# Kernel optimization log

Measured on AMD Instinct MI355X. Metric: run time of the kernel, lower is better.

Reference implementation:

```python
import jax, jax.numpy as jnp
import numpy as np

D = 192   # token_dim == channel_dim == expert_dim == adapt_dim (required by source code)
S = 4096  # sequence length
NE = 8    # num_experts


def _ln(x, g, b, eps=1e-5):
    m = x.mean(-1, keepdims=True)
    v = ((x - m) ** 2).mean(-1, keepdims=True)
    return (x - m) / jnp.sqrt(v + eps) * g + b


def _adaptive(x, a, W, b, AW, Ab):
    # AdaptiveLinear with adapt_method='add': weight = W + adapt(a).view(out, in)
    dW = (AW @ a + Ab).reshape(W.shape)
    return x @ (W + dW).T + b


def setup_inputs() -> dict:
    key = jax.random.key(0)
    ks = iter(jax.random.split(key, 40))

    def n(shape, s=0.05):
        return jax.random.normal(next(ks), shape, dtype=jnp.float32) * s

    return {
        "x": n((1, S, D), 1.0),
        "W_in": n((D, D)), "b_in": n((D,)),
        "feat_W": n((D, D)), "feat_b": n((D,)),
        "feat_AW": n((D * D, D)), "feat_Ab": n((D * D,)),
        "an_g": jnp.ones((D,)), "an_b": jnp.zeros((D,)),
        "tm_W": n((D, D)), "tm_b": n((D,)),
        "tm_AW": n((D * D, D)), "tm_Ab": n((D * D,)),
        "tn_g": jnp.ones((D,)), "tn_b": jnp.zeros((D,)),
        "cm_W": n((D, D)), "cm_b": n((D,)),
        "cm_AW": n((D * D, D)), "cm_Ab": n((D * D,)),
        "cn_g": jnp.ones((D,)), "cn_b": jnp.zeros((D,)),
        "pm_W": n((D, D)), "pm_b": n((D,)),
        "gate_W": n((NE, D)), "gate_b": n((NE,)),
        "ex_W": n((NE, D, D)), "ex_b": n((NE, D)),
        "ex_AW": n((NE, D * D, D)), "ex_Ab": n((NE, D * D)),
        "mn_g": jnp.ones((D,)), "mn_b": jnp.zeros((D,)),
        "out_W": n((D, D)), "out_b": n((D,)),
    }


def reference(x, W_in, b_in, feat_W, feat_b, feat_AW, feat_Ab, an_g, an_b,
              tm_W, tm_b, tm_AW, tm_Ab, tn_g, tn_b,
              cm_W, cm_b, cm_AW, cm_Ab, cn_g, cn_b,
              pm_W, pm_b, gate_W, gate_b, ex_W, ex_b, ex_AW, ex_Ab,
              mn_g, mn_b, out_W, out_b):
    h = x @ W_in.T + b_in                                        # [1,S,D]
    xm = h.mean(axis=1)                                          # [1,D]
    a = _adaptive(xm, xm[0], feat_W, feat_b, feat_AW, feat_Ab)   # [1,D]
    a = _ln(a, an_g, an_b)
    a0 = a[0]                                                    # [D]
    t = _adaptive(h, a0, tm_W, tm_b, tm_AW, tm_Ab)               # token mixing
    t = _ln(t, tn_g, tn_b)
    c = _adaptive(t, a0, cm_W, cm_b, cm_AW, cm_Ab)               # channel mixing
    c = _ln(c, cn_g, cn_b)
    m = c @ pm_W.T + pm_b                                        # pre-MoE [1,S,D]
    gate = jax.nn.softmax(a @ gate_W.T + gate_b, axis=-1)[0]     # [NE]
    # batched hypernet weight generation for all experts at once
    dW = (jnp.einsum('eka,a->ek', ex_AW, a0) + ex_Ab).reshape(NE, D, D)
    We = ex_W + dW                                               # [NE,D,D]
    ye = jnp.einsum('bsd,ned->nbse', m, We) + ex_b[:, None, None, :]
    eo = jnp.einsum('n,nbse->bse', gate, ye)                     # soft-MoE sum
    eo = _ln(eo, mn_g, mn_b)
    eo = jax.nn.relu(eo)
    return eo @ out_W.T + out_b
```

## Files before the change

### kernel.cpp

```cpp
#include <hip/hip_runtime.h>

#define DD 192

template <int EMIT, int LNL>
__global__ __launch_bounds__(256) void stage3_k(
    const float* __restrict__ A, const float* __restrict__ W,
    const float* __restrict__ bias,
    const float* __restrict__ stats_in, const float* __restrict__ lng,
    const float* __restrict__ lnb,
    float* __restrict__ out, float* __restrict__ emit_buf) {
    __shared__ float At[32 * 200];
    __shared__ float WT[DD * 64];
    __shared__ float ms[32], rs[32];
    __shared__ float csum[4 * 64];

    const int t = threadIdx.x;
    const int tr = t >> 5, tc = t & 31;
    const int b = blockIdx.x;
    const int cg = b % 3;
    const int c0 = cg * 64;
    const int r0 = (b / 3) * 32;

    if (LNL > 0) {
        if (t < 32) {
            int r = r0 + t;
            float s = stats_in[2 * r] + stats_in[8192 + 2 * r] + stats_in[16384 + 2 * r];
            float q = stats_in[2 * r + 1] + stats_in[8192 + 2 * r + 1]
                    + stats_in[16384 + 2 * r + 1];
            float mean = s * (1.f / 192.f);
            float var = q * (1.f / 192.f) - mean * mean;
            ms[t] = mean;
            rs[t] = rsqrtf(var + 1e-5f);
        }
        __syncthreads();
    }

    {
        const float4* A4 = (const float4*)(A + (size_t)r0 * DD);
#pragma unroll
        for (int q = 0; q < 6; q++) {
            int f = t + 256 * q;
            int r = f / 48, jj = f - r * 48;
            float4 v = A4[f];
            if (LNL > 0) {
                float mean = ms[r], rstd = rs[r];
                float4 g4 = ((const float4*)lng)[jj];
                float4 b4 = ((const float4*)lnb)[jj];
                v.x = (v.x - mean) * rstd * g4.x + b4.x;
                v.y = (v.y - mean) * rstd * g4.y + b4.y;
                v.z = (v.z - mean) * rstd * g4.z + b4.z;
                v.w = (v.w - mean) * rstd * g4.w + b4.w;
                if (LNL == 2) {
                    v.x = fmaxf(v.x, 0.f); v.y = fmaxf(v.y, 0.f);
                    v.z = fmaxf(v.z, 0.f); v.w = fmaxf(v.w, 0.f);
                }
            }
            *(float4*)&At[r * 200 + 4 * jj] = v;
        }
    }
    {
        const float4* W4 = (const float4*)(W + (size_t)c0 * DD);
#pragma unroll
        for (int q = 0; q < 12; q++) {
            int f = t + 256 * q;
            int ip = f / 48, jj = f - ip * 48;
            float4 v = W4[f];
            int j0 = 4 * jj;
            WT[(j0 + 0) * 64 + ((ip + 2 * ((j0 + 0) & 31)) & 63)] = v.x;
            WT[(j0 + 1) * 64 + ((ip + 2 * ((j0 + 1) & 31)) & 63)] = v.y;
            WT[(j0 + 2) * 64 + ((ip + 2 * ((j0 + 2) & 31)) & 63)] = v.z;
            WT[(j0 + 3) * 64 + ((ip + 2 * ((j0 + 3) & 31)) & 63)] = v.w;
        }
    }

    const int i0 = c0 + 2 * tc;
    float bv0 = bias[i0], bv1 = bias[i0 + 1];
    float acc[4][2];
#pragma unroll
    for (int i = 0; i < 4; i++) { acc[i][0] = bv0; acc[i][1] = bv1; }
    __syncthreads();

    const int rbase = 4 * tr;
#pragma unroll 4
    for (int j = 0; j < DD; j++) {
        int cs = (2 * tc + 2 * (j & 31)) & 63;
        float2 w2 = *(const float2*)&WT[j * 64 + cs];
        float a0 = At[(rbase + 0) * 200 + j];
        float a1 = At[(rbase + 1) * 200 + j];
        float a2 = At[(rbase + 2) * 200 + j];
        float a3 = At[(rbase + 3) * 200 + j];
        acc[0][0] = fmaf(a0, w2.x, acc[0][0]); acc[0][1] = fmaf(a0, w2.y, acc[0][1]);
        acc[1][0] = fmaf(a1, w2.x, acc[1][0]); acc[1][1] = fmaf(a1, w2.y, acc[1][1]);
        acc[2][0] = fmaf(a2, w2.x, acc[2][0]); acc[2][1] = fmaf(a2, w2.y, acc[2][1]);
        acc[3][0] = fmaf(a3, w2.x, acc[3][0]); acc[3][1] = fmaf(a3, w2.y, acc[3][1]);
    }

#pragma unroll
    for (int i = 0; i < 4; i++) {
        int row = r0 + rbase + i;
        *(float2*)&out[(size_t)row * DD + i0] = make_float2(acc[i][0], acc[i][1]);
    }

    if (EMIT == 2) {
#pragma unroll
        for (int i = 0; i < 4; i++) {
            float s = acc[i][0] + acc[i][1];
            float q = acc[i][0] * acc[i][0] + acc[i][1] * acc[i][1];
#pragma unroll
            for (int m = 16; m >= 1; m >>= 1) {
                s += __shfl_xor(s, m);
                q += __shfl_xor(q, m);
            }
            if (tc == 0) {
                int r = r0 + rbase + i;
                emit_buf[cg * 8192 + 2 * r] = s;
                emit_buf[cg * 8192 + 2 * r + 1] = q;
            }
        }
    } else if (EMIT == 1) {
        float cs0 = acc[0][0] + acc[1][0] + acc[2][0] + acc[3][0];
        float cs1 = acc[0][1] + acc[1][1] + acc[2][1] + acc[3][1];
        cs0 += __shfl_xor(cs0, 32);
        cs1 += __shfl_xor(cs1, 32);
        int w = t >> 6;
        if ((t & 63) < 32) {
            csum[w * 64 + 2 * tc] = cs0;
            csum[w * 64 + 2 * tc + 1] = cs1;
        }
        __syncthreads();
        if (t < 64) {
            float s = csum[t] + csum[64 + t] + csum[128 + t] + csum[192 + t];
            atomicAdd(&emit_buf[c0 + t], s);
        }
    }
}

__global__ __launch_bounds__(256) void hyper_k(
    const float* __restrict__ tm_W, const float* __restrict__ tm_AW,
    const float* __restrict__ tm_Ab, const float* __restrict__ cm_W,
    const float* __restrict__ cm_AW, const float* __restrict__ cm_Ab,
    const float* __restrict__ ex_W, const float* __restrict__ ex_AW,
    const float* __restrict__ ex_Ab, const float* __restrict__ a0g,
    const float* __restrict__ gateg, float* __restrict__ Wt,
    float* __restrict__ Wc, float* __restrict__ Wmoe) {
    __shared__ float a0s[DD];
    __shared__ float rows[32 * 204];
    __shared__ float wb[32], ab[32], vals[32];
    const int t = threadIdx.x;
    const int b = blockIdx.x;
    const float* AW; const float* WB; const float* AB;
    int k0, mode, e = 0;
    if (b < 1152)      { mode = 0; AW = tm_AW; WB = tm_W; AB = tm_Ab; k0 = b * 32; }
    else if (b < 2304) { mode = 1; AW = cm_AW; WB = cm_W; AB = cm_Ab; k0 = (b - 1152) * 32; }
    else {
        mode = 2; int bb = b - 2304; e = bb / 1152; k0 = (bb - e * 1152) * 32;
        AW = ex_AW + (size_t)e * 36864 * DD;
        WB = ex_W + (size_t)e * 36864;
        AB = ex_Ab + (size_t)e * 36864;
    }
    if (t < DD) a0s[t] = a0g[t];
    if (t < 32) { wb[t] = WB[k0 + t]; ab[t] = AB[k0 + t]; }
    const float4* src4 = (const float4*)(AW + (size_t)k0 * DD);
#pragma unroll
    for (int q = 0; q < 6; q++) {
        int fidx = t + 256 * q;
        int r = fidx / 48, jj = fidx - r * 48;
        float4 v = src4[fidx];
        *(float4*)&rows[r * 204 + 4 * jj] = v;
    }
    __syncthreads();
    const int r = t >> 3, p = t & 7;
    float acc = 0.f;
#pragma unroll
    for (int q = 0; q < 6; q++) {
        int jo = p * 24 + 4 * q;
        float4 w = *(const float4*)&rows[r * 204 + jo];
        float4 aa = *(const float4*)&a0s[jo];
        acc = fmaf(w.x, aa.x, acc); acc = fmaf(w.y, aa.y, acc);
        acc = fmaf(w.z, aa.z, acc); acc = fmaf(w.w, aa.w, acc);
    }
    acc += __shfl_xor(acc, 1);
    acc += __shfl_xor(acc, 2);
    acc += __shfl_xor(acc, 4);
    if (p == 0) vals[r] = acc + wb[r] + ab[r];
    __syncthreads();
    if (t < 32) {
        if (mode == 0) Wt[k0 + t] = vals[t];
        else if (mode == 1) Wc[k0 + t] = vals[t];
        else atomicAdd(&Wmoe[k0 + t], gateg[e] * vals[t]);
    }
}

__global__ __launch_bounds__(256) void feat2_k(
    const float* __restrict__ feat_W, const float* __restrict__ feat_AW,
    const float* __restrict__ feat_Ab, const float* __restrict__ xm_sum,
    float* __restrict__ a_pre) {
    __shared__ float xms[DD];
    __shared__ float rows[32 * 204];
    __shared__ float wb[32], ab[32], vals[32];
    const int t = threadIdx.x;
    const int k0 = blockIdx.x * 32;
    if (t < DD) xms[t] = xm_sum[t] * (1.f / 4096.f);
    if (t < 32) { wb[t] = feat_W[k0 + t]; ab[t] = feat_Ab[k0 + t]; }
    const float4* src4 = (const float4*)(feat_AW + (size_t)k0 * DD);
#pragma unroll
    for (int q = 0; q < 6; q++) {
        int fidx = t + 256 * q;
        int r = fidx / 48, jj = fidx - r * 48;
        float4 v = src4[fidx];
        *(float4*)&rows[r * 204 + 4 * jj] = v;
    }
    __syncthreads();
    const int r = t >> 3, p = t & 7;
    float acc = 0.f;
#pragma unroll
    for (int q = 0; q < 6; q++) {
        int jo = p * 24 + 4 * q;
        float4 w = *(const float4*)&rows[r * 204 + jo];
        float4 aa = *(const float4*)&xms[jo];
        acc = fmaf(w.x, aa.x, acc); acc = fmaf(w.y, aa.y, acc);
        acc = fmaf(w.z, aa.z, acc); acc = fmaf(w.w, aa.w, acc);
    }
    acc += __shfl_xor(acc, 1);
    acc += __shfl_xor(acc, 2);
    acc += __shfl_xor(acc, 4);
    if (p == 0) vals[r] = acc + wb[r] + ab[r];
    __syncthreads();
    const int j0 = k0 % DD;
    if (t < 32) {
        float c = vals[t] * xms[j0 + t];
#pragma unroll
        for (int m = 16; m >= 1; m >>= 1) c += __shfl_xor(c, m);
        if (t == 0) atomicAdd(&a_pre[k0 / DD], c);
    }
}

__global__ __launch_bounds__(192) void vec_k(
    const float* __restrict__ a_pre, const float* __restrict__ feat_b,
    const float* __restrict__ an_g, const float* __restrict__ an_b,
    const float* __restrict__ gate_W, const float* __restrict__ gate_b,
    const float* __restrict__ ex_b, float* __restrict__ a0g,
    float* __restrict__ gateg, float* __restrict__ b_moe) {
    __shared__ float lgs[8];
    __shared__ float red[6];
    const int t = threadIdx.x;
    float v = a_pre[t] + feat_b[t];
    float s = v, q = v * v;
#pragma unroll
    for (int m = 32; m >= 1; m >>= 1) {
        s += __shfl_xor(s, m);
        q += __shfl_xor(q, m);
    }
    if ((t & 63) == 0) { red[t >> 6] = s; red[3 + (t >> 6)] = q; }
    if (t < 8) lgs[t] = gate_b[t];
    __syncthreads();
    float S = red[0] + red[1] + red[2];
    float Q = red[3] + red[4] + red[5];
    float mean = S * (1.f / 192.f);
    float var = Q * (1.f / 192.f) - mean * mean;
    float rstd = rsqrtf(var + 1e-5f);
    float a0v = (v - mean) * rstd * an_g[t] + an_b[t];
    a0g[t] = a0v;
#pragma unroll
    for (int e = 0; e < 8; e++) atomicAdd(&lgs[e], a0v * gate_W[e * DD + t]);
    __syncthreads();
    if (t == 0) {
        float mx = lgs[0];
        for (int e = 1; e < 8; e++) mx = fmaxf(mx, lgs[e]);
        float sum = 0.f, ex[8];
        for (int e = 0; e < 8; e++) { ex[e] = expf(lgs[e] - mx); sum += ex[e]; }
        for (int e = 0; e < 8; e++) lgs[e] = ex[e] / sum;
    }
    __syncthreads();
    if (t < 8) gateg[t] = lgs[t];
    float bm = 0.f;
#pragma unroll
    for (int e = 0; e < 8; e++) bm = fmaf(lgs[e], ex_b[e * DD + t], bm);
    b_moe[t] = bm;
}

extern "C" void kernel_launch(void* const* d_in, const int* in_sizes, int n_in,
                              void* d_out, int out_size, void* d_ws, size_t ws_size,
                              hipStream_t stream) {
    (void)in_sizes; (void)n_in; (void)out_size; (void)ws_size;
    const float* x       = (const float*)d_in[0];
    const float* W_in    = (const float*)d_in[1];
    const float* b_in    = (const float*)d_in[2];
    const float* feat_W  = (const float*)d_in[3];
    const float* feat_b  = (const float*)d_in[4];
    const float* feat_AW = (const float*)d_in[5];
    const float* feat_Ab = (const float*)d_in[6];
    const float* an_g    = (const float*)d_in[7];
    const float* an_b    = (const float*)d_in[8];
    const float* tm_W    = (const float*)d_in[9];
    const float* tm_b    = (const float*)d_in[10];
    const float* tm_AW   = (const float*)d_in[11];
    const float* tm_Ab   = (const float*)d_in[12];
    const float* tn_g    = (const float*)d_in[13];
    const float* tn_b    = (const float*)d_in[14];
    const float* cm_W    = (const float*)d_in[15];
    const float* cm_b    = (const float*)d_in[16];
    const float* cm_AW   = (const float*)d_in[17];
    const float* cm_Ab   = (const float*)d_in[18];
    const float* cn_g    = (const float*)d_in[19];
    const float* cn_b    = (const float*)d_in[20];
    const float* pm_W    = (const float*)d_in[21];
    const float* pm_b    = (const float*)d_in[22];
    const float* gate_W  = (const float*)d_in[23];
    const float* gate_b  = (const float*)d_in[24];
    const float* ex_W    = (const float*)d_in[25];
    const float* ex_b    = (const float*)d_in[26];
    const float* ex_AW   = (const float*)d_in[27];
    const float* ex_Ab   = (const float*)d_in[28];
    const float* mn_g    = (const float*)d_in[29];
    const float* mn_b    = (const float*)d_in[30];
    const float* out_W   = (const float*)d_in[31];
    const float* out_b   = (const float*)d_in[32];

    float* ws = (float*)d_ws;
    float* B0     = ws;
    float* B1     = ws + 786432;
    float* xm_sum = ws + 1572864;
    float* a_pre  = ws + 1573056;
    float* Wmoe   = ws + 1573248;
    float* Wt     = ws + 1610112;
    float* Wc     = ws + 1646976;
    float* st1    = ws + 1683840;
    float* st2    = ws + 1708416;
    float* st3    = ws + 1732992;
    float* a0     = ws + 1757568;
    float* gate   = ws + 1757760;
    float* b_moe  = ws + 1757768;

    hipMemsetAsync(xm_sum, 0, (size_t)37248 * sizeof(float), stream);

    stage3_k<1, 0><<<384, 256, 0, stream>>>(x, W_in, b_in, nullptr, nullptr, nullptr,
                                            B0, xm_sum);
    feat2_k<<<1152, 256, 0, stream>>>(feat_W, feat_AW, feat_Ab, xm_sum, a_pre);
    vec_k<<<1, 192, 0, stream>>>(a_pre, feat_b, an_g, an_b, gate_W, gate_b, ex_b,
                                 a0, gate, b_moe);
    hyper_k<<<11520, 256, 0, stream>>>(tm_W, tm_AW, tm_Ab, cm_W, cm_AW, cm_Ab,
                                       ex_W, ex_AW, ex_Ab, a0, gate, Wt, Wc, Wmoe);
    stage3_k<2, 0><<<384, 256, 0, stream>>>(B0, Wt, tm_b, nullptr, nullptr, nullptr,
                                            B1, st1);
    stage3_k<2, 1><<<384, 256, 0, stream>>>(B1, Wc, cm_b, st1, tn_g, tn_b, B0, st2);
    stage3_k<0, 1><<<384, 256, 0, stream>>>(B0, pm_W, pm_b, st2, cn_g, cn_b, B1, nullptr);
    stage3_k<2, 0><<<384, 256, 0, stream>>>(B1, Wmoe, b_moe, nullptr, nullptr, nullptr,
                                            B0, st3);
    stage3_k<0, 2><<<384, 256, 0, stream>>>(B0, out_W, out_b, st3, mn_g, mn_b,
                                            (float*)d_out, nullptr);
}
```

Before: 537.8 us.

## Fold expert hypernet loop into one block per slice, drop atomics and big memset

The hypernetwork kernel now gives each block one 32-element slice and loops over all 8 experts, accumulating the gated sum in registers. It then writes Wmoe directly instead of issuing per-expert global atomics, so Wmoe no longer needs zeroing and the memset shrinks to the small accumulators. The stage GEMM inner loop loads activations as float4 vectors in chunks of 8, and the gate logits use wave shuffles instead of shared-memory atomics. The cost is fewer, longer blocks streaming the large ex_AW tensor (3456 blocks instead of 11520), which reduces memory-level parallelism per block.

```diff
diff --git a/kernel.cpp b/kernel.cpp
--- a/kernel.cpp
+++ b/kernel.cpp
@@ -81,18 +81,30 @@
     __syncthreads();
 
     const int rbase = 4 * tr;
-#pragma unroll 4
-    for (int j = 0; j < DD; j++) {
-        int cs = (2 * tc + 2 * (j & 31)) & 63;
-        float2 w2 = *(const float2*)&WT[j * 64 + cs];
-        float a0 = At[(rbase + 0) * 200 + j];
-        float a1 = At[(rbase + 1) * 200 + j];
-        float a2 = At[(rbase + 2) * 200 + j];
-        float a3 = At[(rbase + 3) * 200 + j];
-        acc[0][0] = fmaf(a0, w2.x, acc[0][0]); acc[0][1] = fmaf(a0, w2.y, acc[0][1]);
-        acc[1][0] = fmaf(a1, w2.x, acc[1][0]); acc[1][1] = fmaf(a1, w2.y, acc[1][1]);
-        acc[2][0] = fmaf(a2, w2.x, acc[2][0]); acc[2][1] = fmaf(a2, w2.y, acc[2][1]);
-        acc[3][0] = fmaf(a3, w2.x, acc[3][0]); acc[3][1] = fmaf(a3, w2.y, acc[3][1]);
+#pragma unroll 2
+    for (int jc = 0; jc < DD; jc += 8) {
+        float a_[4][8];
+#pragma unroll
+        for (int rr = 0; rr < 4; rr++) {
+            float4 u = *(const float4*)&At[(rbase + rr) * 200 + jc];
+            float4 v = *(const float4*)&At[(rbase + rr) * 200 + jc + 4];
+            a_[rr][0] = u.x; a_[rr][1] = u.y; a_[rr][2] = u.z; a_[rr][3] = u.w;
+            a_[rr][4] = v.x; a_[rr][5] = v.y; a_[rr][6] = v.z; a_[rr][7] = v.w;
+        }
+#pragma unroll
+        for (int jj = 0; jj < 8; jj++) {
+            const int j = jc + jj;
+            int cs = (2 * tc + 2 * (j & 31)) & 63;
+            float2 w2 = *(const float2*)&WT[j * 64 + cs];
+            acc[0][0] = fmaf(a_[0][jj], w2.x, acc[0][0]);
+            acc[0][1] = fmaf(a_[0][jj], w2.y, acc[0][1]);
+            acc[1][0] = fmaf(a_[1][jj], w2.x, acc[1][0]);
+            acc[1][1] = fmaf(a_[1][jj], w2.y, acc[1][1]);
+            acc[2][0] = fmaf(a_[2][jj], w2.x, acc[2][0]);
+            acc[2][1] = fmaf(a_[2][jj], w2.y, acc[2][1]);
+            acc[3][0] = fmaf(a_[3][jj], w2.x, acc[3][0]);
+            acc[3][1] = fmaf(a_[3][jj], w2.y, acc[3][1]);
+        }
     }
 
 #pragma unroll
@@ -146,48 +158,77 @@
     __shared__ float a0s[DD];
     __shared__ float rows[32 * 204];
     __shared__ float wb[32], ab[32], vals[32];
+    __shared__ float gs[8];
     const int t = threadIdx.x;
     const int b = blockIdx.x;
-    const float* AW; const float* WB; const float* AB;
-    int k0, mode, e = 0;
-    if (b < 1152)      { mode = 0; AW = tm_AW; WB = tm_W; AB = tm_Ab; k0 = b * 32; }
-    else if (b < 2304) { mode = 1; AW = cm_AW; WB = cm_W; AB = cm_Ab; k0 = (b - 1152) * 32; }
-    else {
-        mode = 2; int bb = b - 2304; e = bb / 1152; k0 = (bb - e * 1152) * 32;
-        AW = ex_AW + (size_t)e * 36864 * DD;
-        WB = ex_W + (size_t)e * 36864;
-        AB = ex_Ab + (size_t)e * 36864;
-    }
+    const int r = t >> 3, p = t & 7;
     if (t < DD) a0s[t] = a0g[t];
-    if (t < 32) { wb[t] = WB[k0 + t]; ab[t] = AB[k0 + t]; }
-    const float4* src4 = (const float4*)(AW + (size_t)k0 * DD);
-#pragma unroll
-    for (int q = 0; q < 6; q++) {
-        int fidx = t + 256 * q;
-        int r = fidx / 48, jj = fidx - r * 48;
-        float4 v = src4[fidx];
-        *(float4*)&rows[r * 204 + 4 * jj] = v;
-    }
-    __syncthreads();
-    const int r = t >> 3, p = t & 7;
-    float acc = 0.f;
-#pragma unroll
-    for (int q = 0; q < 6; q++) {
-        int jo = p * 24 + 4 * q;
-        float4 w = *(const float4*)&rows[r * 204 + jo];
-        float4 aa = *(const float4*)&a0s[jo];
-        acc = fmaf(w.x, aa.x, acc); acc = fmaf(w.y, aa.y, acc);
-        acc = fmaf(w.z, aa.z, acc); acc = fmaf(w.w, aa.w, acc);
-    }
-    acc += __shfl_xor(acc, 1);
-    acc += __shfl_xor(acc, 2);
-    acc += __shfl_xor(acc, 4);
-    if (p == 0) vals[r] = acc + wb[r] + ab[r];
-    __syncthreads();
-    if (t < 32) {
-        if (mode == 0) Wt[k0 + t] = vals[t];
-        else if (mode == 1) Wc[k0 + t] = vals[t];
-        else atomicAdd(&Wmoe[k0 + t], gateg[e] * vals[t]);
+
+    if (b < 2304) {
+        const float* AW; const float* WB; const float* AB; float* dst;
+        int k0;
+        if (b < 1152) { AW = tm_AW; WB = tm_W; AB = tm_Ab; dst = Wt; k0 = b * 32; }
+        else          { AW = cm_AW; WB = cm_W; AB = cm_Ab; dst = Wc; k0 = (b - 1152) * 32; }
+        if (t < 32) { wb[t] = WB[k0 + t]; ab[t] = AB[k0 + t]; }
+        const float4* src4 = (const float4*)(AW + (size_t)k0 * DD);
+#pragma unroll
+        for (int q = 0; q < 6; q++) {
+            int fidx = t + 256 * q;
+            int rr = fidx / 48, jj = fidx - rr * 48;
+            *(float4*)&rows[rr * 204 + 4 * jj] = src4[fidx];
+        }
+        __syncthreads();
+        float acc = 0.f;
+#pragma unroll
+        for (int q = 0; q < 6; q++) {
+            int jo = p * 24 + 4 * q;
+            float4 w = *(const float4*)&rows[r * 204 + jo];
+            float4 aa = *(const float4*)&a0s[jo];
+            acc = fmaf(w.x, aa.x, acc); acc = fmaf(w.y, aa.y, acc);
+            acc = fmaf(w.z, aa.z, acc); acc = fmaf(w.w, aa.w, acc);
+        }
+        acc += __shfl_xor(acc, 1);
+        acc += __shfl_xor(acc, 2);
+        acc += __shfl_xor(acc, 4);
+        if (p == 0) vals[r] = acc + wb[r] + ab[r];
+        __syncthreads();
+        if (t < 32) dst[k0 + t] = vals[t];
+    } else {
+        const int k0 = (b - 2304) * 32;
+        if (t < 8) gs[t] = gateg[t];
+        float macc = 0.f;
+        for (int e = 0; e < 8; e++) {
+            __syncthreads();
+            const float4* src4 =
+                (const float4*)(ex_AW + (size_t)e * 36864 * DD + (size_t)k0 * DD);
+#pragma unroll
+            for (int q = 0; q < 6; q++) {
+                int fidx = t + 256 * q;
+                int rr = fidx / 48, jj = fidx - rr * 48;
+                *(float4*)&rows[rr * 204 + 4 * jj] = src4[fidx];
+            }
+            __syncthreads();
+            float acc = 0.f;
+#pragma unroll
+            for (int q = 0; q < 6; q++) {
+                int jo = p * 24 + 4 * q;
+                float4 w = *(const float4*)&rows[r * 204 + jo];
+                float4 aa = *(const float4*)&a0s[jo];
+                acc = fmaf(w.x, aa.x, acc); acc = fmaf(w.y, aa.y, acc);
+                acc = fmaf(w.z, aa.z, acc); acc = fmaf(w.w, aa.w, acc);
+            }
+            acc += __shfl_xor(acc, 1);
+            acc += __shfl_xor(acc, 2);
+            acc += __shfl_xor(acc, 4);
+            if (p == 0) vals[r] = acc;
+            __syncthreads();
+            if (t < 32) {
+                float we = ex_W[(size_t)e * 36864 + k0 + t];
+                float ae = ex_Ab[(size_t)e * 36864 + k0 + t];
+                macc = fmaf(gs[e], vals[t] + we + ae, macc);
+            }
+        }
+        if (t < 32) Wmoe[k0 + t] = macc;
     }
 }
 
@@ -241,9 +282,11 @@
     const float* __restrict__ gate_W, const float* __restrict__ gate_b,
     const float* __restrict__ ex_b, float* __restrict__ a0g,
     float* __restrict__ gateg, float* __restrict__ b_moe) {
+    __shared__ float red[6];
+    __shared__ float gred[24];
     __shared__ float lgs[8];
-    __shared__ float red[6];
     const int t = threadIdx.x;
+    const int w = t >> 6;
     float v = a_pre[t] + feat_b[t];
     float s = v, q = v * v;
 #pragma unroll
@@ -251,8 +294,7 @@
         s += __shfl_xor(s, m);
         q += __shfl_xor(q, m);
     }
-    if ((t & 63) == 0) { red[t >> 6] = s; red[3 + (t >> 6)] = q; }
-    if (t < 8) lgs[t] = gate_b[t];
+    if ((t & 63) == 0) { red[w] = s; red[3 + w] = q; }
     __syncthreads();
     float S = red[0] + red[1] + red[2];
     float Q = red[3] + red[4] + red[5];
@@ -262,7 +304,14 @@
     float a0v = (v - mean) * rstd * an_g[t] + an_b[t];
     a0g[t] = a0v;
 #pragma unroll
-    for (int e = 0; e < 8; e++) atomicAdd(&lgs[e], a0v * gate_W[e * DD + t]);
+    for (int e = 0; e < 8; e++) {
+        float x = a0v * gate_W[e * DD + t];
+#pragma unroll
+        for (int m = 32; m >= 1; m >>= 1) x += __shfl_xor(x, m);
+        if ((t & 63) == 0) gred[w * 8 + e] = x;
+    }
+    __syncthreads();
+    if (t < 8) lgs[t] = gred[t] + gred[8 + t] + gred[16 + t] + gate_b[t];
     __syncthreads();
     if (t == 0) {
         float mx = lgs[0];
@@ -332,15 +381,15 @@
     float* gate   = ws + 1757760;
     float* b_moe  = ws + 1757768;
 
-    hipMemsetAsync(xm_sum, 0, (size_t)37248 * sizeof(float), stream);
+    hipMemsetAsync(xm_sum, 0, (size_t)384 * sizeof(float), stream);
 
     stage3_k<1, 0><<<384, 256, 0, stream>>>(x, W_in, b_in, nullptr, nullptr, nullptr,
                                             B0, xm_sum);
     feat2_k<<<1152, 256, 0, stream>>>(feat_W, feat_AW, feat_Ab, xm_sum, a_pre);
     vec_k<<<1, 192, 0, stream>>>(a_pre, feat_b, an_g, an_b, gate_W, gate_b, ex_b,
                                  a0, gate, b_moe);
-    hyper_k<<<11520, 256, 0, stream>>>(tm_W, tm_AW, tm_Ab, cm_W, cm_AW, cm_Ab,
-                                       ex_W, ex_AW, ex_Ab, a0, gate, Wt, Wc, Wmoe);
+    hyper_k<<<3456, 256, 0, stream>>>(tm_W, tm_AW, tm_Ab, cm_W, cm_AW, cm_Ab,
+                                      ex_W, ex_AW, ex_Ab, a0, gate, Wt, Wc, Wmoe);
     stage3_k<2, 0><<<384, 256, 0, stream>>>(B0, Wt, tm_b, nullptr, nullptr, nullptr,
                                             B1, st1);
     stage3_k<2, 1><<<384, 256, 0, stream>>>(B1, Wc, cm_b, st1, tn_g, tn_b, B0, st2);
```

Measured after the change: 532.5 us. Within noise of the previous version (-1.0%).

## Read pre-transposed weights from global into registers instead of LDS staging

Applied to the files above, without the earlier changes.

Weights for the row-wise GEMM stages are stored transposed (via a new transpose kernel and transposed hyper_k writes) so each thread streams its weight pairs directly from global memory with register prefetching. This removes the per-block LDS weight transpose, halves the row tile to 16, and doubles the grid to raise occupancy. The gate-logit reduction in vec_k switches from shared atomics to warp shuffles. The cost is strided scattered stores and atomics in hyper_k, plus more repeated global weight reads per block.

```diff
diff --git a/kernel.cpp b/kernel.cpp
--- a/kernel.cpp
+++ b/kernel.cpp
@@ -1,28 +1,38 @@
 #include <hip/hip_runtime.h>
 
 #define DD 192
+
+__global__ __launch_bounds__(256) void tr3_k(
+    const float* __restrict__ W_in, const float* __restrict__ pm_W,
+    const float* __restrict__ out_W, float* __restrict__ WinT,
+    float* __restrict__ pmT, float* __restrict__ outT) {
+    int g = blockIdx.x * 256 + threadIdx.x;
+    int m = g / 36864, e = g - m * 36864;
+    int i = e / DD, j = e - i * DD;
+    const float* s = (m == 0) ? W_in : (m == 1) ? pm_W : out_W;
+    float* d = (m == 0) ? WinT : (m == 1) ? pmT : outT;
+    d[(size_t)j * DD + i] = s[e];
+}
 
 template <int EMIT, int LNL>
 __global__ __launch_bounds__(256) void stage3_k(
-    const float* __restrict__ A, const float* __restrict__ W,
+    const float* __restrict__ A, const float* __restrict__ WTg,
     const float* __restrict__ bias,
     const float* __restrict__ stats_in, const float* __restrict__ lng,
     const float* __restrict__ lnb,
     float* __restrict__ out, float* __restrict__ emit_buf) {
-    __shared__ float At[32 * 200];
-    __shared__ float WT[DD * 64];
-    __shared__ float ms[32], rs[32];
-    __shared__ float csum[4 * 64];
+    __shared__ float At[16 * 200];
+    __shared__ float ms[16], rs[16];
+    __shared__ float csum[256];
 
     const int t = threadIdx.x;
     const int tr = t >> 5, tc = t & 31;
     const int b = blockIdx.x;
-    const int cg = b % 3;
-    const int c0 = cg * 64;
-    const int r0 = (b / 3) * 32;
+    const int cg = b % 3, c0 = cg * 64;
+    const int r0 = (b / 3) * 16;
 
     if (LNL > 0) {
-        if (t < 32) {
+        if (t < 16) {
             int r = r0 + t;
             float s = stats_in[2 * r] + stats_in[8192 + 2 * r] + stats_in[16384 + 2 * r];
             float q = stats_in[2 * r + 1] + stats_in[8192 + 2 * r + 1]
@@ -38,7 +48,7 @@
     {
         const float4* A4 = (const float4*)(A + (size_t)r0 * DD);
 #pragma unroll
-        for (int q = 0; q < 6; q++) {
+        for (int q = 0; q < 3; q++) {
             int f = t + 256 * q;
             int r = f / 48, jj = f - r * 48;
             float4 v = A4[f];
@@ -58,52 +68,71 @@
             *(float4*)&At[r * 200 + 4 * jj] = v;
         }
     }
+
+    const int i0 = c0 + 2 * tc;
+    const float* wp = WTg + i0;
+    float bv0 = bias[i0], bv1 = bias[i0 + 1];
+    float acc[2][2];
+#pragma unroll
+    for (int i = 0; i < 2; i++) { acc[i][0] = bv0; acc[i][1] = bv1; }
+    float2 wreg[8];
+#pragma unroll
+    for (int jj = 0; jj < 8; jj++) wreg[jj] = *(const float2*)(wp + jj * DD);
+    __syncthreads();
+
+    const int rbase = 2 * tr;
+#pragma unroll 2
+    for (int jc = 0; jc < DD - 8; jc += 8) {
+        float2 wcur[8];
+#pragma unroll
+        for (int jj = 0; jj < 8; jj++) wcur[jj] = wreg[jj];
+#pragma unroll
+        for (int jj = 0; jj < 8; jj++)
+            wreg[jj] = *(const float2*)(wp + (jc + 8 + jj) * DD);
+        float a_[2][8];
+#pragma unroll
+        for (int rr = 0; rr < 2; rr++) {
+            float4 u = *(const float4*)&At[(rbase + rr) * 200 + jc];
+            float4 v = *(const float4*)&At[(rbase + rr) * 200 + jc + 4];
+            a_[rr][0] = u.x; a_[rr][1] = u.y; a_[rr][2] = u.z; a_[rr][3] = u.w;
+            a_[rr][4] = v.x; a_[rr][5] = v.y; a_[rr][6] = v.z; a_[rr][7] = v.w;
+        }
+#pragma unroll
+        for (int jj = 0; jj < 8; jj++) {
+            acc[0][0] = fmaf(a_[0][jj], wcur[jj].x, acc[0][0]);
+            acc[0][1] = fmaf(a_[0][jj], wcur[jj].y, acc[0][1]);
+            acc[1][0] = fmaf(a_[1][jj], wcur[jj].x, acc[1][0]);
+            acc[1][1] = fmaf(a_[1][jj], wcur[jj].y, acc[1][1]);
+        }
+    }
     {
-        const float4* W4 = (const float4*)(W + (size_t)c0 * DD);
-#pragma unroll
-        for (int q = 0; q < 12; q++) {
-            int f = t + 256 * q;
-            int ip = f / 48, jj = f - ip * 48;
-            float4 v = W4[f];
-            int j0 = 4 * jj;
-            WT[(j0 + 0) * 64 + ((ip + 2 * ((j0 + 0) & 31)) & 63)] = v.x;
-            WT[(j0 + 1) * 64 + ((ip + 2 * ((j0 + 1) & 31)) & 63)] = v.y;
-            WT[(j0 + 2) * 64 + ((ip + 2 * ((j0 + 2) & 31)) & 63)] = v.z;
-            WT[(j0 + 3) * 64 + ((ip + 2 * ((j0 + 3) & 31)) & 63)] = v.w;
-        }
-    }
-
-    const int i0 = c0 + 2 * tc;
-    float bv0 = bias[i0], bv1 = bias[i0 + 1];
-    float acc[4][2];
-#pragma unroll
-    for (int i = 0; i < 4; i++) { acc[i][0] = bv0; acc[i][1] = bv1; }
-    __syncthreads();
-
-    const int rbase = 4 * tr;
-#pragma unroll 4
-    for (int j = 0; j < DD; j++) {
-        int cs = (2 * tc + 2 * (j & 31)) & 63;
-        float2 w2 = *(const float2*)&WT[j * 64 + cs];
-        float a0 = At[(rbase + 0) * 200 + j];
-        float a1 = At[(rbase + 1) * 200 + j];
-        float a2 = At[(rbase + 2) * 200 + j];
-        float a3 = At[(rbase + 3) * 200 + j];
-        acc[0][0] = fmaf(a0, w2.x, acc[0][0]); acc[0][1] = fmaf(a0, w2.y, acc[0][1]);
-        acc[1][0] = fmaf(a1, w2.x, acc[1][0]); acc[1][1] = fmaf(a1, w2.y, acc[1][1]);
-        acc[2][0] = fmaf(a2, w2.x, acc[2][0]); acc[2][1] = fmaf(a2, w2.y, acc[2][1]);
-        acc[3][0] = fmaf(a3, w2.x, acc[3][0]); acc[3][1] = fmaf(a3, w2.y, acc[3][1]);
-    }
-
-#pragma unroll
-    for (int i = 0; i < 4; i++) {
+        const int jc = DD - 8;
+        float a_[2][8];
+#pragma unroll
+        for (int rr = 0; rr < 2; rr++) {
+            float4 u = *(const float4*)&At[(rbase + rr) * 200 + jc];
+            float4 v = *(const float4*)&At[(rbase + rr) * 200 + jc + 4];
+            a_[rr][0] = u.x; a_[rr][1] = u.y; a_[rr][2] = u.z; a_[rr][3] = u.w;
+            a_[rr][4] = v.x; a_[rr][5] = v.y; a_[rr][6] = v.z; a_[rr][7] = v.w;
+        }
+#pragma unroll
+        for (int jj = 0; jj < 8; jj++) {
+            acc[0][0] = fmaf(a_[0][jj], wreg[jj].x, acc[0][0]);
+            acc[0][1] = fmaf(a_[0][jj], wreg[jj].y, acc[0][1]);
+            acc[1][0] = fmaf(a_[1][jj], wreg[jj].x, acc[1][0]);
+            acc[1][1] = fmaf(a_[1][jj], wreg[jj].y, acc[1][1]);
+        }
+    }
+
+#pragma unroll
+    for (int i = 0; i < 2; i++) {
         int row = r0 + rbase + i;
         *(float2*)&out[(size_t)row * DD + i0] = make_float2(acc[i][0], acc[i][1]);
     }
 
     if (EMIT == 2) {
 #pragma unroll
-        for (int i = 0; i < 4; i++) {
+        for (int i = 0; i < 2; i++) {
             float s = acc[i][0] + acc[i][1];
             float q = acc[i][0] * acc[i][0] + acc[i][1] * acc[i][1];
 #pragma unroll
@@ -118,8 +147,8 @@
             }
         }
     } else if (EMIT == 1) {
-        float cs0 = acc[0][0] + acc[1][0] + acc[2][0] + acc[3][0];
-        float cs1 = acc[0][1] + acc[1][1] + acc[2][1] + acc[3][1];
+        float cs0 = acc[0][0] + acc[1][0];
+        float cs1 = acc[0][1] + acc[1][1];
         cs0 += __shfl_xor(cs0, 32);
         cs1 += __shfl_xor(cs1, 32);
         int w = t >> 6;
@@ -141,8 +170,8 @@
     const float* __restrict__ cm_AW, const float* __restrict__ cm_Ab,
     const float* __restrict__ ex_W, const float* __restrict__ ex_AW,
     const float* __restrict__ ex_Ab, const float* __restrict__ a0g,
-    const float* __restrict__ gateg, float* __restrict__ Wt,
-    float* __restrict__ Wc, float* __restrict__ Wmoe) {
+    const float* __restrict__ gateg, float* __restrict__ WtT,
+    float* __restrict__ WcT, float* __restrict__ WmoeT) {
     __shared__ float a0s[DD];
     __shared__ float rows[32 * 204];
     __shared__ float wb[32], ab[32], vals[32];
@@ -165,8 +194,7 @@
     for (int q = 0; q < 6; q++) {
         int fidx = t + 256 * q;
         int r = fidx / 48, jj = fidx - r * 48;
-        float4 v = src4[fidx];
-        *(float4*)&rows[r * 204 + 4 * jj] = v;
+        *(float4*)&rows[r * 204 + 4 * jj] = src4[fidx];
     }
     __syncthreads();
     const int r = t >> 3, p = t & 7;
@@ -185,9 +213,10 @@
     if (p == 0) vals[r] = acc + wb[r] + ab[r];
     __syncthreads();
     if (t < 32) {
-        if (mode == 0) Wt[k0 + t] = vals[t];
-        else if (mode == 1) Wc[k0 + t] = vals[t];
-        else atomicAdd(&Wmoe[k0 + t], gateg[e] * vals[t]);
+        int i = k0 / DD, jb = k0 - i * DD;
+        if (mode == 0) WtT[(size_t)(jb + t) * DD + i] = vals[t];
+        else if (mode == 1) WcT[(size_t)(jb + t) * DD + i] = vals[t];
+        else atomicAdd(&WmoeT[(size_t)(jb + t) * DD + i], gateg[e] * vals[t]);
     }
 }
 
@@ -207,8 +236,7 @@
     for (int q = 0; q < 6; q++) {
         int fidx = t + 256 * q;
         int r = fidx / 48, jj = fidx - r * 48;
-        float4 v = src4[fidx];
-        *(float4*)&rows[r * 204 + 4 * jj] = v;
+        *(float4*)&rows[r * 204 + 4 * jj] = src4[fidx];
     }
     __syncthreads();
     const int r = t >> 3, p = t & 7;
@@ -241,18 +269,16 @@
     const float* __restrict__ gate_W, const float* __restrict__ gate_b,
     const float* __restrict__ ex_b, float* __restrict__ a0g,
     float* __restrict__ gateg, float* __restrict__ b_moe) {
+    __shared__ float red[6];
+    __shared__ float gred[24];
     __shared__ float lgs[8];
-    __shared__ float red[6];
     const int t = threadIdx.x;
+    const int w = t >> 6;
     float v = a_pre[t] + feat_b[t];
     float s = v, q = v * v;
 #pragma unroll
-    for (int m = 32; m >= 1; m >>= 1) {
-        s += __shfl_xor(s, m);
-        q += __shfl_xor(q, m);
-    }
-    if ((t & 63) == 0) { red[t >> 6] = s; red[3 + (t >> 6)] = q; }
-    if (t < 8) lgs[t] = gate_b[t];
+    for (int m = 32; m >= 1; m >>= 1) { s += __shfl_xor(s, m); q += __shfl_xor(q, m); }
+    if ((t & 63) == 0) { red[w] = s; red[3 + w] = q; }
     __syncthreads();
     float S = red[0] + red[1] + red[2];
     float Q = red[3] + red[4] + red[5];
@@ -262,7 +288,14 @@
     float a0v = (v - mean) * rstd * an_g[t] + an_b[t];
     a0g[t] = a0v;
 #pragma unroll
-    for (int e = 0; e < 8; e++) atomicAdd(&lgs[e], a0v * gate_W[e * DD + t]);
+    for (int e = 0; e < 8; e++) {
+        float x = a0v * gate_W[e * DD + t];
+#pragma unroll
+        for (int m = 32; m >= 1; m >>= 1) x += __shfl_xor(x, m);
+        if ((t & 63) == 0) gred[w * 8 + e] = x;
+    }
+    __syncthreads();
+    if (t < 8) lgs[t] = gred[t] + gred[8 + t] + gred[16 + t] + gate_b[t];
     __syncthreads();
     if (t == 0) {
         float mx = lgs[0];
@@ -322,31 +355,35 @@
     float* B1     = ws + 786432;
     float* xm_sum = ws + 1572864;
     float* a_pre  = ws + 1573056;
-    float* Wmoe   = ws + 1573248;
-    float* Wt     = ws + 1610112;
-    float* Wc     = ws + 1646976;
+    float* WmoeT  = ws + 1573248;
+    float* WtT    = ws + 1610112;
+    float* WcT    = ws + 1646976;
     float* st1    = ws + 1683840;
     float* st2    = ws + 1708416;
     float* st3    = ws + 1732992;
     float* a0     = ws + 1757568;
     float* gate   = ws + 1757760;
     float* b_moe  = ws + 1757768;
+    float* WinT   = ws + 1758208;
+    float* pmT    = ws + 1795072;
+    float* outT   = ws + 1831936;
 
     hipMemsetAsync(xm_sum, 0, (size_t)37248 * sizeof(float), stream);
 
-    stage3_k<1, 0><<<384, 256, 0, stream>>>(x, W_in, b_in, nullptr, nullptr, nullptr,
+    tr3_k<<<432, 256, 0, stream>>>(W_in, pm_W, out_W, WinT, pmT, outT);
+    stage3_k<1, 0><<<768, 256, 0, stream>>>(x, WinT, b_in, nullptr, nullptr, nullptr,
                                             B0, xm_sum);
     feat2_k<<<1152, 256, 0, stream>>>(feat_W, feat_AW, feat_Ab, xm_sum, a_pre);
     vec_k<<<1, 192, 0, stream>>>(a_pre, feat_b, an_g, an_b, gate_W, gate_b, ex_b,
                                  a0, gate, b_moe);
     hyper_k<<<11520, 256, 0, stream>>>(tm_W, tm_AW, tm_Ab, cm_W, cm_AW, cm_Ab,
-                                       ex_W, ex_AW, ex_Ab, a0, gate, Wt, Wc, Wmoe);
-    stage3_k<2, 0><<<384, 256, 0, stream>>>(B0, Wt, tm_b, nullptr, nullptr, nullptr,
+                                       ex_W, ex_AW, ex_Ab, a0, gate, WtT, WcT, WmoeT);
+    stage3_k<2, 0><<<768, 256, 0, stream>>>(B0, WtT, tm_b, nullptr, nullptr, nullptr,
                                             B1, st1);
-    stage3_k<2, 1><<<384, 256, 0, stream>>>(B1, Wc, cm_b, st1, tn_g, tn_b, B0, st2);
-    stage3_k<0, 1><<<384, 256, 0, stream>>>(B0, pm_W, pm_b, st2, cn_g, cn_b, B1, nullptr);
-    stage3_k<2, 0><<<384, 256, 0, stream>>>(B1, Wmoe, b_moe, nullptr, nullptr, nullptr,
+    stage3_k<2, 1><<<768, 256, 0, stream>>>(B1, WcT, cm_b, st1, tn_g, tn_b, B0, st2);
+    stage3_k<0, 1><<<768, 256, 0, stream>>>(B0, pmT, pm_b, st2, cn_g, cn_b, B1, nullptr);
+    stage3_k<2, 0><<<768, 256, 0, stream>>>(B1, WmoeT, b_moe, nullptr, nullptr, nullptr,
                                             B0, st3);
-    stage3_k<0, 2><<<384, 256, 0, stream>>>(B0, out_W, out_b, st3, mn_g, mn_b,
+    stage3_k<0, 2><<<768, 256, 0, stream>>>(B0, outT, out_b, st3, mn_g, mn_b,
                                             (float*)d_out, nullptr);
 }
```

Result: slower. 559.3 us (+4.0%).
